# Kernel optimization log

Measured on AMD Instinct MI355X. Metric: run time of the kernel, lower is better.

The kernel has to match this reference:

```python
import jax, jax.numpy as jnp
import numpy as np

BLOCK_SIZE = 8
SELECT_TOPK = 32
HIDDEN = 512
CHANNELS = 384
NUM_HEADS = 8
B, H, W = 8, 64, 64


def setup_inputs() -> dict:
    key = jax.random.key(0)
    ks = jax.random.split(key, 8)
    num_block_tot = (H // BLOCK_SIZE) * (W // BLOCK_SIZE)
    bs2 = BLOCK_SIZE * BLOCK_SIZE
    x = jax.random.normal(ks[0], (B, H, W, CHANNELS), dtype=jnp.float32)
    aw = jax.random.normal(ks[1], (NUM_HEADS, B, num_block_tot, bs2, bs2 + SELECT_TOPK), dtype=jnp.float32)
    attn_weights = jax.nn.softmax(aw, axis=-1)  # module expects sum(-1)==1
    weights = jax.random.uniform(ks[2], (B, num_block_tot, SELECT_TOPK), dtype=jnp.float32)
    indexes = jax.random.randint(ks[3], (B, num_block_tot, SELECT_TOPK), 0, H * W)
    in_proj_w = jax.random.normal(ks[4], (3 * HIDDEN, CHANNELS), dtype=jnp.float32) * 0.02
    in_proj_b = jax.random.normal(ks[5], (3 * HIDDEN,), dtype=jnp.float32) * 0.02
    out_proj_w = jax.random.normal(ks[6], (CHANNELS, HIDDEN), dtype=jnp.float32) * 0.02
    out_proj_b = jax.random.normal(ks[7], (CHANNELS,), dtype=jnp.float32) * 0.02
    return {"x": x, "attn_weights": attn_weights, "weights": weights,
            "in_proj_w": in_proj_w, "in_proj_b": in_proj_b,
            "out_proj_w": out_proj_w, "out_proj_b": out_proj_b,
            "indexes": indexes}


def reference(x, attn_weights, weights, in_proj_w, in_proj_b, out_proj_w, out_proj_b, indexes):
    batch, height, width, _ = x.shape
    bsz = BLOCK_SIZE
    nbh, nbw = height // bsz, width // bsz
    nbt = nbh * nbw
    num_heads = attn_weights.shape[0]
    hid = HIDDEN
    hd = hid // num_heads
    topk = SELECT_TOPK

    proj = jnp.einsum('bhwc,oc->bhwo', x, in_proj_w) + in_proj_b  # (B,H,W,3*hid)
    s, xh, y = jnp.split(proj, 3, axis=-1)
    xh = xh * jnp.tanh(s)  # Balancer/Whiten/Identity are identity in fwd

    # top-k gathered tokens: (B, nbt, topk, hid) without (B,nbt,num_tokens,hid) blowup
    x_flat = xh.reshape(batch, height * width, hid)
    sel = jax.vmap(lambda xf, ix: xf[ix])(x_flat, indexes)  # (B,nbt,topk,hid)
    sel = sel * weights[..., None]
    sel = sel.reshape(batch, nbt, topk, num_heads, hd).transpose(3, 0, 1, 2, 4)  # (nh,B,nbt,topk,hd)

    # block-local tokens: (nh, B, nbt, bsz^2, hd)
    blk = xh.reshape(batch, nbh, bsz, nbw, bsz, num_heads, hd)
    blk = blk.transpose(5, 0, 1, 3, 2, 4, 6).reshape(num_heads, batch, nbt, bsz * bsz, hd)

    kv = jnp.concatenate([blk, sel], axis=3)  # (nh,B,nbt,bsz^2+topk,hd)
    out = jnp.einsum('hbnqk,hbnkd->hbnqd', attn_weights, kv)  # (nh,B,nbt,bsz^2,hd)

    out = out.reshape(num_heads, batch, nbh, nbw, bsz, bsz, hd)
    out = out.transpose(1, 2, 4, 3, 5, 0, 6).reshape(batch, height, width, hid)
    out = out * y
    return jnp.einsum('bhwd,cd->bhwc', out, out_proj_w) + out_proj_b
```

## Files before the change

### kernel.cpp

```cpp
#include <hip/hip_runtime.h>
#include <hip/hip_bf16.h>
#include <stdint.h>

#define CH   384
#define HID  512
#define NHD  8
#define MTOT 32768

typedef __attribute__((ext_vector_type(8))) short bf16x8;
typedef __attribute__((ext_vector_type(4))) float f32x4;
typedef unsigned short u16;

__device__ __forceinline__ float bf2f(u16 v){ return __uint_as_float(((unsigned)v)<<16); }
__device__ __forceinline__ u16 f2bf(float f){
  unsigned u = __float_as_uint(f);
  return (u16)((u + 0x7fffu + ((u>>16)&1u)) >> 16);
}
__device__ __forceinline__ float fast_tanh(float s){
  float e = __expf(2.f*s);
  return 1.f - 2.f*__builtin_amdgcn_rcpf(e + 1.f);
}
__device__ __forceinline__ void gload_lds16(const void* g, void* l){
  __builtin_amdgcn_global_load_lds((const __attribute__((address_space(1))) void*)g,
                                   (__attribute__((address_space(3))) void*)l, 16, 0, 0);
}

#define CVT_N1 (MTOT*CH/4)
#define CVT_N2 (3*HID*CH/4)
#define CVT_N3 (CH*HID/4)
__global__ void k_cvt3(const float* __restrict__ x,  u16* __restrict__ xo,
                       const float* __restrict__ w1, u16* __restrict__ w1o,
                       const float* __restrict__ w2, u16* __restrict__ w2o){
  const int total = CVT_N1 + CVT_N2 + CVT_N3;
  int i = blockIdx.x*blockDim.x + threadIdx.x;
  int stride = gridDim.x*blockDim.x;
  for (; i < total; i += stride){
    const float4* src; ushort4* dst; int k;
    if (i < CVT_N1){ src = (const float4*)x;  dst = (ushort4*)xo;  k = i; }
    else if (i < CVT_N1 + CVT_N2){ src = (const float4*)w1; dst = (ushort4*)w1o; k = i - CVT_N1; }
    else { src = (const float4*)w2; dst = (ushort4*)w2o; k = i - CVT_N1 - CVT_N2; }
    float4 v = src[k];
    ushort4 o; o.x=f2bf(v.x); o.y=f2bf(v.y); o.z=f2bf(v.z); o.w=f2bf(v.w);
    dst[k] = o;
  }
}

__global__ __launch_bounds__(256)
void k_gemm1(const u16* __restrict__ xb, const u16* __restrict__ w1b,
             const float* __restrict__ b1,
             u16* __restrict__ xh, u16* __restrict__ yb)
{
  __shared__ short lds[14336];
  const int tid = threadIdx.x;
  const int w = tid >> 6, lw = tid & 63;
  const int bid = blockIdx.x;
  const int xcd = bid & 7, ii = bid >> 3;
  const int m0 = (xcd*32 + (ii >> 4)) * 128;
  const int h0 = (ii & 15) * 32;
  const int lc = lw & 15, lk = lw >> 4;

  f32x4 acc[2][6] = {};

  const int sl = (lw & 7) ^ (lw >> 3);
  const int rsub = lw >> 3;
  const u16* gsrc[7]; int ldst[7];
  #pragma unroll
  for (int i = 0; i < 7; ++i){
    int c = w*7 + i;
    if (c < 16){
      int r = c*8 + rsub;
      gsrc[i] = xb + (size_t)(m0 + r)*CH + sl*8;
      ldst[i] = c*512;
    } else {
      int rb = (c-16)*8 + rsub;
      int grow = (rb >> 5)*HID + h0 + (rb & 31);
      gsrc[i] = w1b + (size_t)grow*CH + sl*8;
      ldst[i] = 8192 + (c-16)*512;
    }
  }

  #pragma unroll 1
  for (int kt = 0; kt < 6; ++kt){
    #pragma unroll
    for (int i = 0; i < 7; ++i)
      gload_lds16(gsrc[i] + kt*64, &lds[ldst[i]]);
    __syncthreads();
    #pragma unroll
    for (int ks = 0; ks < 2; ++ks){
      const int s = (ks*4 + lk) ^ (lc & 7);
      bf16x8 af[2], bfr[6];
      #pragma unroll
      for (int mi = 0; mi < 2; ++mi){
        int row = w*32 + mi*16 + lc;
        af[mi] = *(const bf16x8*)&lds[row*64 + s*8];
      }
      #pragma unroll
      for (int nj = 0; nj < 6; ++nj){
        int row = nj*16 + lc;
        bfr[nj] = *(const bf16x8*)&lds[8192 + row*64 + s*8];
      }
      #pragma unroll
      for (int mi = 0; mi < 2; ++mi)
        #pragma unroll
        for (int nj = 0; nj < 6; ++nj)
          acc[mi][nj] = __builtin_amdgcn_mfma_f32_16x16x32_bf16(af[mi], bfr[nj], acc[mi][nj], 0,0,0);
    }
    __syncthreads();
  }

  {
    short* epx = &lds[w*2560];
    short* epy = &lds[w*2560 + 1280];
    float bs[2], bx[2], by[2];
    #pragma unroll
    for (int f = 0; f < 2; ++f){
      int col = h0 + f*16 + lc;
      bs[f] = b1[col]; bx[f] = b1[512 + col]; by[f] = b1[1024 + col];
    }
    #pragma unroll
    for (int mi = 0; mi < 2; ++mi)
      #pragma unroll
      for (int f = 0; f < 2; ++f)
        #pragma unroll
        for (int j = 0; j < 4; ++j){
          float sv = acc[mi][0+f][j] + bs[f];
          float xv = (acc[mi][2+f][j] + bx[f]) * fast_tanh(sv);
          float yv = acc[mi][4+f][j] + by[f];
          int row = mi*16 + lk*4 + j;
          epx[row*40 + f*16 + lc] = (short)f2bf(xv);
          epy[row*40 + f*16 + lc] = (short)f2bf(yv);
        }
    __syncthreads();
    const int row = lw >> 1, half = lw & 1;
    const size_t gbase = (size_t)(m0 + w*32 + row)*HID + h0 + half*16;
    #pragma unroll
    for (int q = 0; q < 2; ++q){
      bf16x8 v = *(const bf16x8*)&epx[row*40 + half*16 + q*8];
      *(bf16x8*)&xh[gbase + q*8] = v;
    }
    #pragma unroll
    for (int q = 0; q < 2; ++q){
      bf16x8 v = *(const bf16x8*)&epy[row*40 + half*16 + q*8];
      *(bf16x8*)&yb[gbase + q*8] = v;
    }
  }
}

__global__ __launch_bounds__(64, 3)
void k_attn(const float* __restrict__ aw, const float* __restrict__ wts,
            const int* __restrict__ idxs,
            const u16* __restrict__ xh, const u16* __restrict__ yb,
            u16* __restrict__ zb)
{
  __shared__ short ldsb[6144 + 12288];
  short* lKv = ldsb;
  float* lAw = (float*)&ldsb[6144];
  const int tid = threadIdx.x;
  const int bid = blockIdx.x;
  const int h = bid >> 9;
  const int b = (bid >> 6) & 7;
  const int n = bid & 63;
  const int bh = n >> 3, bw = n & 7;

  {
    const float* awt = aw + (size_t)bid * 6144;
    #pragma unroll
    for (int i = 0; i < 24; ++i){
      int s = i*64 + tid;
      int row = s / 24;
      int sir = s - row*24;
      int src = row*24 + (sir ^ (row & 7));
      gload_lds16(awt + src*4, (char*)lAw + (size_t)i*1024);
    }
  }

  {
    const int dg = tid & 7;
    const int pr = tid >> 3;
    #pragma unroll
    for (int it = 0; it < 6; ++it){
      int pair = it*8 + pr;
      int t0 = pair*2;
      size_t r0, r1;
      if (t0 < 64){
        int pix = (bh*8 + (t0>>3))*64 + bw*8 + (t0&7);
        r0 = (size_t)b*4096 + pix;
        r1 = r0 + 1;
      } else {
        int e = (b*64+n)*32 + (t0-64);
        r0 = (size_t)b*4096 + idxs[e];
        r1 = (size_t)b*4096 + idxs[e+1];
      }
      bf16x8 v0 = *(const bf16x8*)&xh[r0*HID + h*64 + dg*8];
      bf16x8 v1 = *(const bf16x8*)&xh[r1*HID + h*64 + dg*8];
      #pragma unroll
      for (int j = 0; j < 8; ++j){
        int d = dg*8 + j;
        int elem = (d*96 + t0) ^ (dg<<3);
        unsigned pk = (unsigned)(u16)v0[j] | ((unsigned)(u16)v1[j] << 16);
        *(unsigned*)&lKv[elem] = pk;
      }
    }
  }

  float wv[8];
  {
    const float* wp = wts + (size_t)(b*64+n)*32 + (tid>>4)*8;
    float4 a = *(const float4*)wp, c = *(const float4*)(wp+4);
    wv[0]=a.x; wv[1]=a.y; wv[2]=a.z; wv[3]=a.w;
    wv[4]=c.x; wv[5]=c.y; wv[6]=c.z; wv[7]=c.w;
  }
  bf16x8 yv[8];
  {
    int pix = (bh*8 + (tid>>3))*64 + bw*8 + (tid&7);
    const u16* yrow = yb + ((size_t)b*4096 + pix)*HID + h*64;
    #pragma unroll
    for (int c = 0; c < 8; ++c)
      yv[c] = *(const bf16x8*)&yrow[c*8];
  }
  __syncthreads();

  const int lc = tid & 15, lk = tid >> 4;
  f32x4 acc[4][4] = {};
  #pragma unroll
  for (int ks = 0; ks < 3; ++ks){
    bf16x8 af[4];
    #pragma unroll
    for (int mi = 0; mi < 4; ++mi){
      int r = mi*16 + lc;
      int sr = ks*8 + lk*2;
      int key = r & 7;
      float4 f0 = *(const float4*)&lAw[(r*24 + (sr ^ key))*4];
      float4 f1 = *(const float4*)&lAw[(r*24 + ((sr+1) ^ key))*4];
      float t[8] = {f0.x,f0.y,f0.z,f0.w,f1.x,f1.y,f1.z,f1.w};
      #pragma unroll
      for (int j = 0; j < 8; ++j){
        float v = (ks == 2) ? t[j]*wv[j] : t[j];
        af[mi][j] = (short)f2bf(v);
      }
    }
    bf16x8 bv[4];
    #pragma unroll
    for (int nj = 0; nj < 4; ++nj){
      int d = nj*16 + lc;
      int idx = (d*96 + ks*32 + lk*8) ^ ((d>>3)<<3);
      bv[nj] = *(const bf16x8*)&lKv[idx];
    }
    #pragma unroll
    for (int mi = 0; mi < 4; ++mi)
      #pragma unroll
      for (int nj = 0; nj < 4; ++nj)
        acc[mi][nj] = __builtin_amdgcn_mfma_f32_16x16x32_bf16(af[mi], bv[nj], acc[mi][nj], 0,0,0);
  }

  {
    const int q = tid;
    #pragma unroll
    for (int c = 0; c < 8; ++c)
      *(bf16x8*)&lKv[q*72 + c*8] = yv[c];
  }

  #pragma unroll
  for (int mi = 0; mi < 4; ++mi){
    #pragma unroll
    for (int nj = 0; nj < 4; ++nj){
      int d = nj*16 + lc;
      size_t gcol = (size_t)h*64 + d;
      #pragma unroll
      for (int j = 0; j < 4; ++j){
        int q = mi*16 + lk*4 + j;
        int pix = (bh*8 + (q>>3))*64 + bw*8 + (q&7);
        size_t r = (size_t)b*4096 + pix;
        float yvf = bf2f((u16)lKv[q*72 + d]);
        zb[r*HID + gcol] = f2bf(acc[mi][nj][j] * yvf);
      }
    }
  }
}

__global__ __launch_bounds__(256)
void k_gemm2(const u16* __restrict__ zb, const u16* __restrict__ w2b,
             const float* __restrict__ b2, float* __restrict__ out)
{
  __shared__ short lds[16384];
  const int tid = threadIdx.x;
  const int w = tid>>6, lw = tid&63;
  const int wm = w>>1, wn = w&1;
  const int bid = blockIdx.x;
  const int xcd = bid & 7, ii = bid >> 3;
  const int m0 = (xcd*32 + ii/3) * 128;
  const int n0 = (ii%3) * 128;
  const int lc = lw & 15, lk = lw >> 4;

  f32x4 acc[4][4] = {};

  const int sl_g = (lw & 3) ^ ((lw >> 3) & 3);
  const int rsub = lw >> 2;
  const u16* gsrc[4]; int ldst[4];
  #pragma unroll
  for (int i = 0; i < 4; ++i){
    int c = w*4 + i;
    if (c < 8){
      int r = c*16 + rsub;
      gsrc[i] = zb + (size_t)(m0+r)*HID + sl_g*8;
      ldst[i] = c*512;
    } else {
      int cb = c - 8;
      int r = cb*16 + rsub;
      gsrc[i] = w2b + (size_t)(n0+r)*HID + sl_g*8;
      ldst[i] = 4096 + cb*512;
    }
  }
  auto STAGE = [&](int buf, int kt){
    #pragma unroll
    for (int i = 0; i < 4; ++i)
      gload_lds16(gsrc[i] + kt*32, &lds[ldst[i] + buf*8192]);
  };
  const int skey = (lc >> 1) & 3;
  auto COMPUTE = [&](int buf){
    const short* pa = lds + buf*8192;
    const short* pb = lds + buf*8192 + 4096;
    bf16x8 af[4], bb[4];
    #pragma unroll
    for (int mi=0; mi<4; ++mi){
      int row = wm*64 + mi*16 + lc;
      af[mi] = *(const bf16x8*)&pa[row*32 + (lk ^ skey)*8];
    }
    #pragma unroll
    for (int nj=0; nj<4; ++nj){
      int row = wn*64 + nj*16 + lc;
      bb[nj] = *(const bf16x8*)&pb[row*32 + (lk ^ skey)*8];
    }
    #pragma unroll
    for (int mi=0; mi<4; ++mi)
      #pragma unroll
      for (int nj=0; nj<4; ++nj)
        acc[mi][nj] = __builtin_amdgcn_mfma_f32_16x16x32_bf16(af[mi], bb[nj], acc[mi][nj], 0,0,0);
  };

  STAGE(0, 0);
  #pragma unroll 1
  for (int kt = 0; kt < 16; ++kt){
    if (kt < 15){
      STAGE((kt+1)&1, kt+1);
      asm volatile("s_waitcnt vmcnt(4)" ::: "memory");
    } else {
      asm volatile("s_waitcnt vmcnt(0)" ::: "memory");
    }
    __builtin_amdgcn_sched_barrier(0);
    __builtin_amdgcn_s_barrier();
    COMPUTE(kt&1);
    __builtin_amdgcn_sched_barrier(0);
    __builtin_amdgcn_s_barrier();
  }

  const int lr4 = lk*4;
  #pragma unroll
  for (int nj=0; nj<4; ++nj){
    int col = n0 + wn*64 + nj*16 + lc;
    float bias = b2[col];
    #pragma unroll
    for (int mi=0; mi<4; ++mi){
      #pragma unroll
      for (int j=0; j<4; ++j){
        int row = m0 + wm*64 + mi*16 + lr4 + j;
        out[(size_t)row*CH + col] = acc[mi][nj][j] + bias;
      }
    }
  }
}

extern "C" void kernel_launch(void* const* d_in, const int* in_sizes, int n_in,
                              void* d_out, int out_size, void* d_ws, size_t ws_size,
                              hipStream_t stream) {
  const float* x   = (const float*)d_in[0];
  const float* aw  = (const float*)d_in[1];
  const float* wts = (const float*)d_in[2];
  const float* w1  = (const float*)d_in[3];
  const float* b1  = (const float*)d_in[4];
  const float* w2  = (const float*)d_in[5];
  const float* b2  = (const float*)d_in[6];
  const int*   idx = (const int*)d_in[7];
  float* out = (float*)d_out;

  char* ws = (char*)d_ws;
  u16* x_bf  = (u16*)(ws);
  u16* w1_bf = (u16*)(ws + 25165824);
  u16* w2_bf = (u16*)(ws + 26345472);
  u16* xh_bf = (u16*)(ws + 26738688);
  u16* y_bf  = (u16*)(ws + 60293120);
  u16* z_bf  = (u16*)(ws + 93847552);

  k_cvt3<<<2048, 256, 0, stream>>>(x, x_bf, w1, w1_bf, w2, w2_bf);

  k_gemm1<<<4096, 256, 0, stream>>>(x_bf, w1_bf, b1, xh_bf, y_bf);
  k_attn<<<NHD*8*64, 64, 0, stream>>>(aw, wts, idx, xh_bf, y_bf, z_bf);
  k_gemm2<<<768, 256, 0, stream>>>(z_bf, w2_bf, b2, out);
}
```

Before: 141.0 us.

## Split attention block work across four waves instead of one

The k_attn kernel moves from a single 64-thread wave per (head, batch, block) to 256 threads. Each wave now computes 16 query rows with 4 MFMA accumulators, where one wave previously handled all 64 rows with 16. The aw staging, KV gather and y loads are spread across the four waves, and a barrier is added before y overwrites the KV LDS buffer. The aim is shorter per-block latency and less register pressure, which should give more memory-level parallelism. The cost is one more block-wide sync and larger blocks that may limit how many blocks fit per CU.

```diff
diff --git a/kernel.cpp b/kernel.cpp
--- a/kernel.cpp
+++ b/kernel.cpp
@@ -146,7 +146,7 @@
   }
 }
 
-__global__ __launch_bounds__(64, 3)
+__global__ __launch_bounds__(256)
 void k_attn(const float* __restrict__ aw, const float* __restrict__ wts,
             const int* __restrict__ idxs,
             const u16* __restrict__ xh, const u16* __restrict__ yb,
@@ -155,7 +155,8 @@
   __shared__ short ldsb[6144 + 12288];
   short* lKv = ldsb;
   float* lAw = (float*)&ldsb[6144];
-  const int tid = threadIdx.x;
+  const int tid0 = threadIdx.x;
+  const int w = tid0 >> 6, lane = tid0 & 63;
   const int bid = blockIdx.x;
   const int h = bid >> 9;
   const int b = (bid >> 6) & 7;
@@ -165,32 +166,23 @@
   {
     const float* awt = aw + (size_t)bid * 6144;
     #pragma unroll
-    for (int i = 0; i < 24; ++i){
-      int s = i*64 + tid;
+    for (int i = 0; i < 6; ++i){
+      int c = i*4 + w;
+      int s = c*64 + lane;
       int row = s / 24;
       int sir = s - row*24;
       int src = row*24 + (sir ^ (row & 7));
-      gload_lds16(awt + src*4, (char*)lAw + (size_t)i*1024);
-    }
-  }
-
-  {
-    const int dg = tid & 7;
-    const int pr = tid >> 3;
-    #pragma unroll
-    for (int it = 0; it < 6; ++it){
-      int pair = it*8 + pr;
+      gload_lds16(awt + src*4, (char*)lAw + (size_t)c*1024);
+    }
+  }
+
+  {
+    const int dg = tid0 & 7;
+    {
+      int pair = tid0 >> 3;
       int t0 = pair*2;
-      size_t r0, r1;
-      if (t0 < 64){
-        int pix = (bh*8 + (t0>>3))*64 + bw*8 + (t0&7);
-        r0 = (size_t)b*4096 + pix;
-        r1 = r0 + 1;
-      } else {
-        int e = (b*64+n)*32 + (t0-64);
-        r0 = (size_t)b*4096 + idxs[e];
-        r1 = (size_t)b*4096 + idxs[e+1];
-      }
+      int pix = (bh*8 + (t0>>3))*64 + bw*8 + (t0&7);
+      size_t r0 = (size_t)b*4096 + pix, r1 = r0 + 1;
       bf16x8 v0 = *(const bf16x8*)&xh[r0*HID + h*64 + dg*8];
       bf16x8 v1 = *(const bf16x8*)&xh[r1*HID + h*64 + dg*8];
       #pragma unroll
@@ -201,33 +193,48 @@
         *(unsigned*)&lKv[elem] = pk;
       }
     }
+    if (tid0 < 128){
+      int pr = tid0 >> 3;
+      int t0 = 64 + pr*2;
+      int e = (b*64+n)*32 + pr*2;
+      size_t r0 = (size_t)b*4096 + idxs[e];
+      size_t r1 = (size_t)b*4096 + idxs[e+1];
+      bf16x8 v0 = *(const bf16x8*)&xh[r0*HID + h*64 + dg*8];
+      bf16x8 v1 = *(const bf16x8*)&xh[r1*HID + h*64 + dg*8];
+      #pragma unroll
+      for (int j = 0; j < 8; ++j){
+        int d = dg*8 + j;
+        int elem = (d*96 + t0) ^ (dg<<3);
+        unsigned pk = (unsigned)(u16)v0[j] | ((unsigned)(u16)v1[j] << 16);
+        *(unsigned*)&lKv[elem] = pk;
+      }
+    }
   }
 
   float wv[8];
   {
-    const float* wp = wts + (size_t)(b*64+n)*32 + (tid>>4)*8;
+    const float* wp = wts + (size_t)(b*64+n)*32 + (lane>>4)*8;
     float4 a = *(const float4*)wp, c = *(const float4*)(wp+4);
     wv[0]=a.x; wv[1]=a.y; wv[2]=a.z; wv[3]=a.w;
     wv[4]=c.x; wv[5]=c.y; wv[6]=c.z; wv[7]=c.w;
   }
-  bf16x8 yv[8];
-  {
-    int pix = (bh*8 + (tid>>3))*64 + bw*8 + (tid&7);
-    const u16* yrow = yb + ((size_t)b*4096 + pix)*HID + h*64;
-    #pragma unroll
-    for (int c = 0; c < 8; ++c)
-      yv[c] = *(const bf16x8*)&yrow[c*8];
+  bf16x8 yv0, yv1;
+  const int yq = tid0 >> 2, yc = tid0 & 3;
+  {
+    int pix = (bh*8 + (yq>>3))*64 + bw*8 + (yq&7);
+    const u16* yrow = yb + ((size_t)b*4096 + pix)*HID + h*64 + yc*16;
+    yv0 = *(const bf16x8*)&yrow[0];
+    yv1 = *(const bf16x8*)&yrow[8];
   }
   __syncthreads();
 
-  const int lc = tid & 15, lk = tid >> 4;
-  f32x4 acc[4][4] = {};
+  const int lc = lane & 15, lk = lane >> 4;
+  f32x4 acc[4] = {};
   #pragma unroll
   for (int ks = 0; ks < 3; ++ks){
-    bf16x8 af[4];
-    #pragma unroll
-    for (int mi = 0; mi < 4; ++mi){
-      int r = mi*16 + lc;
+    bf16x8 af;
+    {
+      int r = w*16 + lc;
       int sr = ks*8 + lk*2;
       int key = r & 7;
       float4 f0 = *(const float4*)&lAw[(r*24 + (sr ^ key))*4];
@@ -236,7 +243,7 @@
       #pragma unroll
       for (int j = 0; j < 8; ++j){
         float v = (ks == 2) ? t[j]*wv[j] : t[j];
-        af[mi][j] = (short)f2bf(v);
+        af[j] = (short)f2bf(v);
       }
     }
     bf16x8 bv[4];
@@ -247,33 +254,25 @@
       bv[nj] = *(const bf16x8*)&lKv[idx];
     }
     #pragma unroll
-    for (int mi = 0; mi < 4; ++mi)
-      #pragma unroll
-      for (int nj = 0; nj < 4; ++nj)
-        acc[mi][nj] = __builtin_amdgcn_mfma_f32_16x16x32_bf16(af[mi], bv[nj], acc[mi][nj], 0,0,0);
-  }
-
-  {
-    const int q = tid;
-    #pragma unroll
-    for (int c = 0; c < 8; ++c)
-      *(bf16x8*)&lKv[q*72 + c*8] = yv[c];
-  }
-
-  #pragma unroll
-  for (int mi = 0; mi < 4; ++mi){
-    #pragma unroll
-    for (int nj = 0; nj < 4; ++nj){
-      int d = nj*16 + lc;
-      size_t gcol = (size_t)h*64 + d;
-      #pragma unroll
-      for (int j = 0; j < 4; ++j){
-        int q = mi*16 + lk*4 + j;
-        int pix = (bh*8 + (q>>3))*64 + bw*8 + (q&7);
-        size_t r = (size_t)b*4096 + pix;
-        float yvf = bf2f((u16)lKv[q*72 + d]);
-        zb[r*HID + gcol] = f2bf(acc[mi][nj][j] * yvf);
-      }
+    for (int nj = 0; nj < 4; ++nj)
+      acc[nj] = __builtin_amdgcn_mfma_f32_16x16x32_bf16(af, bv[nj], acc[nj], 0,0,0);
+  }
+  __syncthreads();
+
+  *(bf16x8*)&lKv[yq*72 + yc*16    ] = yv0;
+  *(bf16x8*)&lKv[yq*72 + yc*16 + 8] = yv1;
+
+  #pragma unroll
+  for (int nj = 0; nj < 4; ++nj){
+    int d = nj*16 + lc;
+    size_t gcol = (size_t)h*64 + d;
+    #pragma unroll
+    for (int j = 0; j < 4; ++j){
+      int q = w*16 + lk*4 + j;
+      int pix = (bh*8 + (q>>3))*64 + bw*8 + (q&7);
+      size_t r = (size_t)b*4096 + pix;
+      float yvf = bf2f((u16)lKv[q*72 + d]);
+      zb[r*HID + gcol] = f2bf(acc[nj][j] * yvf);
     }
   }
 }
@@ -394,6 +393,6 @@
   k_cvt3<<<2048, 256, 0, stream>>>(x, x_bf, w1, w1_bf, w2, w2_bf);
 
   k_gemm1<<<4096, 256, 0, stream>>>(x_bf, w1_bf, b1, xh_bf, y_bf);
-  k_attn<<<NHD*8*64, 64, 0, stream>>>(aw, wts, idx, xh_bf, y_bf, z_bf);
+  k_attn<<<NHD*8*64, 256, 0, stream>>>(aw, wts, idx, xh_bf, y_bf, z_bf);
   k_gemm2<<<768, 256, 0, stream>>>(z_bf, w2_bf, b2, out);
 }
```

New measurement: 135.5 us. -3.9%, faster.
